# Optimization experiments

Measured on AMD Instinct MI355X. Metric: run time of the kernel, lower is better.

The kernel has to match this reference:

```python
import jax, jax.numpy as jnp
import numpy as np

NUM_EXPERTS = 8
TOP_K = 2
HIDDEN = 1024
INTER = 2048
SHARED_INTER = 1024
T = 8192
STD = 0.02


def setup_inputs() -> dict:
    key = jax.random.key(0)
    ks = jax.random.split(key, 6)
    return {
        "hidden_states": jax.random.normal(ks[0], (T, HIDDEN), dtype=jnp.float32),
        "w_gate": jax.random.normal(ks[1], (NUM_EXPERTS, HIDDEN), dtype=jnp.float32) * STD,
        "w_fc": jax.random.normal(ks[2], (NUM_EXPERTS, INTER, HIDDEN), dtype=jnp.float32) * STD,
        "w_proj": jax.random.normal(ks[3], (NUM_EXPERTS, HIDDEN, INTER), dtype=jnp.float32) * (STD / np.sqrt(2 * 24)),
        "w_fc_shared": jax.random.normal(ks[4], (SHARED_INTER, HIDDEN), dtype=jnp.float32) * STD,
        "w_proj_shared": jax.random.normal(ks[5], (HIDDEN, SHARED_INTER), dtype=jnp.float32) * (STD / np.sqrt(2 * 24)),
    }


def reference(hidden_states, w_gate, w_fc, w_proj, w_fc_shared, w_proj_shared):
    x = hidden_states.reshape(-1, HIDDEN)  # [T, d]
    # --- routing: top-k over router logits, softmax over the k selected logits (fp32) ---
    router_logits = x @ w_gate.T  # [T, E]
    top_vals, top_idx = jax.lax.top_k(router_logits, TOP_K)  # [T, K]
    gates = jax.nn.softmax(top_vals.astype(jnp.float32), axis=-1).astype(x.dtype)  # [T, K]
    # --- expert FFN: dense per-expert compute, masked combine (== scatter/grouped-GEMM math) ---
    out = jnp.zeros_like(x)
    for e in range(NUM_EXPERTS):
        gate_e = jnp.sum(jnp.where(top_idx == e, gates, jnp.zeros_like(gates)), axis=-1)  # [T]
        h = jax.nn.gelu(x @ w_fc[e].T, approximate=False) @ w_proj[e].T  # [T, d]
        out = out + gate_e[:, None] * h
    # --- shared expert ---
    shared = jax.nn.gelu(x @ w_fc_shared.T, approximate=False) @ w_proj_shared.T
    return out + shared
```

## Files before the change

kernel.cpp:

```cpp
#include <hip/hip_runtime.h>
#include <cstdint>
#include <cstdio>

#define DEVI __device__ __forceinline__

constexpr int TOKS = 8192;
constexpr int HID  = 1024;
constexpr int INTR = 2048;
constexpr int SINT = 1024;
constexpr int NEXP = 8;
constexpr int MAXSLOT = 17408;

typedef __bf16 bf16x8 __attribute__((ext_vector_type(8)));
typedef float  f32x4  __attribute__((ext_vector_type(4)));

DEVI unsigned short f2bf(float f) {
  unsigned int u = __float_as_uint(f);
  u += 0x7FFFu + ((u >> 16) & 1u);
  return (unsigned short)(u >> 16);
}

DEVI float bf2f(unsigned short h) {
  return __uint_as_float((unsigned int)h << 16);
}

DEVI void gl_lds16(const unsigned short* g, unsigned short* l) {
  __attribute__((address_space(1))) uint32_t* gp =
      (__attribute__((address_space(1))) uint32_t*)(uintptr_t)g;
  __attribute__((address_space(3))) uint32_t* lp =
      (__attribute__((address_space(3))) uint32_t*)(uint32_t)(uintptr_t)l;
  __builtin_amdgcn_global_load_lds(gp, lp, 16, 0, 0);
}

DEVI float gelu_fast(float x) {
  const float z = fabsf(x) * 0.70710678118654752f;
  const float t = __builtin_amdgcn_rcpf(1.0f + 0.3275911f * z);
  float p = 1.061405429f;
  p = p * t - 1.453152027f;
  p = p * t + 1.421413741f;
  p = p * t - 0.284496736f;
  p = p * t + 0.254829592f;
  const float e = __builtin_amdgcn_exp2f(-z * z * 1.4426950408889634f);
  float erfz = 1.0f - p * t * e;
  erfz = copysignf(erfz, x);
  return 0.5f * x * (1.0f + erfz);
}

DEVI int xcd_chunk_map(int bid, int total) {
  const int q = total >> 3, r = total & 7;
  const int x = bid & 7, i = bid >> 3;
  return (x < r ? x * (q + 1) : r * (q + 1) + (x - r) * q) + i;
}

__global__ void k_f2bf_all(const float* __restrict__ s0, unsigned short* __restrict__ d0, int n0,
                           const float* __restrict__ s1, unsigned short* __restrict__ d1, int n1,
                           const float* __restrict__ s2, unsigned short* __restrict__ d2, int n2,
                           const float* __restrict__ s3, unsigned short* __restrict__ d3, int n3) {
  const int ntot = n0 + n1 + n2 + n3;
  int i = blockIdx.x * blockDim.x + threadIdx.x;
  const int stride = gridDim.x * blockDim.x;
  for (; i < ntot; i += stride) {
    int j = i;
    const float* s; unsigned short* d;
    if (j < n0) { s = s0; d = d0; }
    else if ((j -= n0) < n1) { s = s1; d = d1; }
    else if ((j -= n1) < n2) { s = s2; d = d2; }
    else { j -= n2; s = s3; d = d3; }
    float4 v = ((const float4*)s)[j];
    ushort4 o;
    o.x = f2bf(v.x); o.y = f2bf(v.y); o.z = f2bf(v.z); o.w = f2bf(v.w);
    ((ushort4*)d)[j] = o;
  }
}

__global__ __launch_bounds__(256) void k_router(
    const float* __restrict__ x, const float* __restrict__ wg,
    unsigned short* __restrict__ xb,
    int* __restrict__ rec_e, float2* __restrict__ rec_g) {
  const int wave = threadIdx.x >> 6;
  const int lane = threadIdx.x & 63;
  const int t = blockIdx.x * 4 + wave;

  float4 xv[4];
  const float4* x4 = (const float4*)(x + (size_t)t * HID);
#pragma unroll
  for (int j = 0; j < 4; ++j) xv[j] = x4[j * 64 + lane];

  ushort4* xb4 = (ushort4*)(xb + (size_t)t * HID);
#pragma unroll
  for (int j = 0; j < 4; ++j) {
    float4 v = xv[j];
    ushort4 o; o.x = f2bf(v.x); o.y = f2bf(v.y); o.z = f2bf(v.z); o.w = f2bf(v.w);
    xb4[j * 64 + lane] = o;
  }

  float lg[NEXP];
#pragma unroll
  for (int e = 0; e < NEXP; ++e) {
    const float4* w4 = (const float4*)(wg + (size_t)e * HID);
    float s = 0.f;
#pragma unroll
    for (int j = 0; j < 4; ++j) {
      float4 a = xv[j], b = w4[j * 64 + lane];
      s += a.x * b.x + a.y * b.y + a.z * b.z + a.w * b.w;
    }
    lg[e] = s;
  }
#pragma unroll
  for (int e = 0; e < NEXP; ++e)
#pragma unroll
    for (int off = 32; off > 0; off >>= 1) lg[e] += __shfl_xor(lg[e], off);

  if (lane == 0) {
    int b0 = 0; float v0 = lg[0];
    for (int e = 1; e < NEXP; ++e) if (lg[e] > v0) { v0 = lg[e]; b0 = e; }
    int b1 = -1; float v1 = -1e30f;
    for (int e = 0; e < NEXP; ++e) if (e != b0 && lg[e] > v1) { v1 = lg[e]; b1 = e; }
    const float d = expf(v1 - v0);
    const float g0 = 1.f / (1.f + d);
    const float g1 = d / (1.f + d);
    rec_e[t] = b0 | (b1 << 16);
    rec_g[t] = make_float2(g0, g1);
  }
}

__global__ __launch_bounds__(256) void k_count(
    const int* __restrict__ rec_e, int* __restrict__ rec_p, int* __restrict__ cnt) {
  __shared__ int hist[NEXP];
  __shared__ int base[NEXP];
  const int t = blockIdx.x * 256 + threadIdx.x;
  if (threadIdx.x < NEXP) hist[threadIdx.x] = 0;
  __syncthreads();
  const int ee = rec_e[t];
  const int e0 = ee & 0xffff, e1 = ee >> 16;
  const int r0 = atomicAdd(&hist[e0], 1);
  const int r1 = atomicAdd(&hist[e1], 1);
  __syncthreads();
  if (threadIdx.x < NEXP)
    base[threadIdx.x] = atomicAdd(&cnt[threadIdx.x], hist[threadIdx.x]);
  __syncthreads();
  rec_p[t] = (base[e0] + r0) | ((base[e1] + r1) << 16);
}

__global__ void k_scan(const int* __restrict__ cnt, int* __restrict__ offs) {
  if (threadIdx.x == 0 && blockIdx.x == 0) {
    int* tb0 = offs + 16;
    int* tb1 = offs + 32;
    int o = 0, t0 = 0, t1 = 0;
    tb0[0] = 0; tb1[0] = 0;
    for (int e = 0; e < NEXP; ++e) {
      offs[e] = o;
      const int mt = (cnt[e] + 127) >> 7;
      o += mt << 7;
      t0 += mt * (INTR / 128);
      t1 += mt * (HID / 128);
      tb0[e + 1] = t0;
      tb1[e + 1] = t1;
    }
    offs[NEXP] = o;
  }
}

__global__ void k_assign(const int* __restrict__ rec_e, const int* __restrict__ rec_p,
                         const int* __restrict__ offs, int* __restrict__ tok) {
  const int t = blockIdx.x * 256 + threadIdx.x;
  if (t >= TOKS) return;
  const int ee = rec_e[t], pp = rec_p[t];
  const int s0 = offs[ee & 0xffff] + (pp & 0xffff);
  const int s1 = offs[ee >> 16] + (pp >> 16);
  tok[s0] = t;
  tok[s1] = t;
}

template <int MODE>
__global__ __launch_bounds__(256, 2) void k_gemm2(
    const unsigned short* __restrict__ A,
    const unsigned short* __restrict__ B,
    unsigned short* __restrict__ Hout,
    const int* __restrict__ cnt,
    const int* __restrict__ offs,
    const int* __restrict__ tok,
    int K, int N) {
  constexpr int NT_SHIFT = (MODE == 0) ? 4 : 3;
  constexpr int NT = 1 << NT_SHIFT;

  int count, off, e = 0, m0, n0;
  {
    int bid = blockIdx.x;
    int total;
    const int* tb = offs + ((MODE == 0) ? 16 : 32);
    if constexpr (MODE <= 1) total = tb[8];
    else                     total = (TOKS >> 7) << NT_SHIFT;
    if (bid >= total) return;
    bid = xcd_chunk_map(bid, total);
    int local;
    if constexpr (MODE <= 1) {
      while (bid >= tb[e + 1]) ++e;
      local = bid - tb[e];
      count = cnt[e]; off = offs[e];
    } else {
      local = bid; count = TOKS; off = 0;
    }
    m0 = (local >> NT_SHIFT) << 7;
    n0 = (local & (NT - 1)) << 7;
  }

  __shared__ alignas(16) unsigned short As[2][128 * 64];
  __shared__ alignas(16) unsigned short Bs[2][128 * 64];

  const int tid = threadIdx.x;
  const unsigned short* Bexp = B + ((MODE <= 1) ? (size_t)e * N * K : (size_t)0);

  const int srow = tid >> 3;
  const int schunk = tid & 7;
  const unsigned short* gA[4];
  const unsigned short* gB[4];
#pragma unroll
  for (int r = 0; r < 4; ++r) {
    const int gr = r * 32 + srow;
    int mr = m0 + gr; if (mr > count - 1) mr = count - 1;
    size_t arow;
    if (MODE == 0)      arow = (size_t)tok[off + mr] * (size_t)K;
    else if (MODE == 1) arow = (size_t)(off + mr) * (size_t)K;
    else                arow = (size_t)(m0 + gr) * (size_t)K;
    gA[r] = A + arow + (size_t)(((schunk ^ (gr & 7)) & 7) * 8);
    gB[r] = Bexp + (size_t)(n0 + gr) * (size_t)K + (size_t)(((schunk ^ (gr & 7)) & 7) * 8);
  }

  const int wid = tid >> 6;
  const int lane = tid & 63;
  const int wr = wid >> 1;
  const int wc = wid & 1;
  const int fm = lane & 15;
  const int fq = lane >> 4;
  int aOff[4], bOff[4];
#pragma unroll
  for (int i = 0; i < 4; ++i) {
    const int row = wr * 64 + i * 16 + fm;
    aOff[i] = row * 128 + ((fq ^ (row & 7)) * 16);
  }
#pragma unroll
  for (int j = 0; j < 4; ++j) {
    const int row = wc * 64 + j * 16 + fm;
    bOff[j] = row * 128 + ((fq ^ (row & 7)) * 16);
  }

  auto stage = [&](int buf, int k0) {
#pragma unroll
    for (int r = 0; r < 4; ++r)
      gl_lds16(gA[r] + k0, &As[buf][r * 2048 + tid * 8]);
#pragma unroll
    for (int r = 0; r < 4; ++r)
      gl_lds16(gB[r] + k0, &Bs[buf][r * 2048 + tid * 8]);
  };

  f32x4 acc[4][4] = {};

  stage(0, 0);
  __syncthreads();

  int cur = 0;
  for (int k0 = 0; k0 < K; k0 += 64) {
    const bool more = (k0 + 64 < K);
    if (more) stage(cur ^ 1, k0 + 64);

    const char* aBase = (const char*)&As[cur][0];
    const char* bBase = (const char*)&Bs[cur][0];
    __builtin_amdgcn_s_setprio(1);
#pragma unroll
    for (int s = 0; s < 2; ++s) {
      bf16x8 af[4], bfr[4];
#pragma unroll
      for (int i = 0; i < 4; ++i)
        af[i] = *(const bf16x8*)(aBase + (aOff[i] ^ (s << 6)));
#pragma unroll
      for (int j = 0; j < 4; ++j)
        bfr[j] = *(const bf16x8*)(bBase + (bOff[j] ^ (s << 6)));
#pragma unroll
      for (int i = 0; i < 4; ++i)
#pragma unroll
        for (int j = 0; j < 4; ++j)
          acc[i][j] = __builtin_amdgcn_mfma_f32_16x16x32_bf16(af[i], bfr[j], acc[i][j], 0, 0, 0);
    }
    __builtin_amdgcn_s_setprio(0);

    if (more) { __syncthreads(); cur ^= 1; }
  }

  constexpr bool GELU = (MODE == 0 || MODE == 2);
#pragma unroll
  for (int i = 0; i < 4; ++i) {
#pragma unroll
    for (int rr = 0; rr < 4; ++rr) {
      const int m = m0 + wr * 64 + i * 16 + fq * 4 + rr;
      if (m < count) {
        unsigned short* orow = Hout + (size_t)(off + m) * N + (n0 + wc * 64 + fm);
#pragma unroll
        for (int j = 0; j < 4; ++j) {
          const float v = acc[i][j][rr];
          orow[j * 16] = f2bf(GELU ? gelu_fast(v) : v);
        }
      }
    }
  }
}

__global__ __launch_bounds__(256) void k_combine(
    const unsigned short* __restrict__ Y,
    const unsigned short* __restrict__ Ys,
    const int* __restrict__ rec_e, const int* __restrict__ rec_p,
    const float2* __restrict__ rec_g, const int* __restrict__ offs,
    float* __restrict__ out) {
  const int t = blockIdx.x;
  const int ee = rec_e[t], pp = rec_p[t];
  const float2 g = rec_g[t];
  const int s0 = offs[ee & 0xffff] + (pp & 0xffff);
  const int s1 = offs[ee >> 16] + (pp >> 16);
  const int c = threadIdx.x * 4;
  ushort4 a = *(const ushort4*)&Y[(size_t)s0 * HID + c];
  ushort4 b = *(const ushort4*)&Y[(size_t)s1 * HID + c];
  ushort4 s = *(const ushort4*)&Ys[(size_t)t * HID + c];
  float4 o;
  o.x = g.x * bf2f(a.x) + g.y * bf2f(b.x) + bf2f(s.x);
  o.y = g.x * bf2f(a.y) + g.y * bf2f(b.y) + bf2f(s.y);
  o.z = g.x * bf2f(a.z) + g.y * bf2f(b.z) + bf2f(s.z);
  o.w = g.x * bf2f(a.w) + g.y * bf2f(b.w) + bf2f(s.w);
  *(float4*)&out[(size_t)t * HID + c] = o;
}

extern "C" void kernel_launch(void* const* d_in, const int* in_sizes, int n_in,
                              void* d_out, int out_size, void* d_ws, size_t ws_size,
                              hipStream_t stream) {
  const float* x   = (const float*)d_in[0];
  const float* wg  = (const float*)d_in[1];
  const float* wfc = (const float*)d_in[2];
  const float* wpj = (const float*)d_in[3];
  const float* wfs = (const float*)d_in[4];
  const float* wps = (const float*)d_in[5];
  float* out = (float*)d_out;
  char* ws = (char*)d_ws;

  constexpr size_t OFF_XB   = 0;
  constexpr size_t OFF_WFC  = OFF_XB   + (size_t)TOKS * HID * 2;
  constexpr size_t OFF_WPJ  = OFF_WFC  + (size_t)NEXP * INTR * HID * 2;
  constexpr size_t OFF_WFS  = OFF_WPJ  + (size_t)NEXP * HID * INTR * 2;
  constexpr size_t OFF_WPS  = OFF_WFS  + (size_t)SINT * HID * 2;
  constexpr size_t OFF_H    = OFF_WPS  + (size_t)HID * SINT * 2;
  constexpr size_t OFF_HS   = OFF_H    + (size_t)MAXSLOT * INTR * 2;
  constexpr size_t OFF_Y    = OFF_HS   + (size_t)TOKS * SINT * 2;
  constexpr size_t OFF_YS   = OFF_Y    + (size_t)MAXSLOT * HID * 2;
  constexpr size_t OFF_CNT  = OFF_YS   + (size_t)TOKS * HID * 2;
  constexpr size_t OFF_OFFS = OFF_CNT  + 32;
  constexpr size_t OFF_RECE = OFF_OFFS + 256;
  constexpr size_t OFF_RECP = OFF_RECE + (size_t)TOKS * 4;
  constexpr size_t OFF_RECG = OFF_RECP + (size_t)TOKS * 4;
  constexpr size_t OFF_TOK  = OFF_RECG + (size_t)TOKS * 8;

  unsigned short* xb   = (unsigned short*)(ws + OFF_XB);
  unsigned short* wfcb = (unsigned short*)(ws + OFF_WFC);
  unsigned short* wpjb = (unsigned short*)(ws + OFF_WPJ);
  unsigned short* wfsb = (unsigned short*)(ws + OFF_WFS);
  unsigned short* wpsb = (unsigned short*)(ws + OFF_WPS);
  unsigned short* h    = (unsigned short*)(ws + OFF_H);
  unsigned short* hs   = (unsigned short*)(ws + OFF_HS);
  unsigned short* Y    = (unsigned short*)(ws + OFF_Y);
  unsigned short* Ys   = (unsigned short*)(ws + OFF_YS);
  int*    cnt   = (int*)(ws + OFF_CNT);
  int*    offs  = (int*)(ws + OFF_OFFS);
  int*    rec_e = (int*)(ws + OFF_RECE);
  int*    rec_p = (int*)(ws + OFF_RECP);
  float2* rec_g = (float2*)(ws + OFF_RECG);
  int*    tok   = (int*)(ws + OFF_TOK);

  hipMemsetAsync(cnt, 0, NEXP * sizeof(int), stream);

  k_f2bf_all<<<2048, 256, 0, stream>>>(
      wfc, wfcb, NEXP * INTR * HID / 4,
      wpj, wpjb, NEXP * HID * INTR / 4,
      wfs, wfsb, SINT * HID / 4,
      wps, wpsb, HID * SINT / 4);

  k_router<<<TOKS / 4, 256, 0, stream>>>(x, wg, xb, rec_e, rec_g);
  k_count<<<TOKS / 256, 256, 0, stream>>>(rec_e, rec_p, cnt);
  k_scan<<<1, 64, 0, stream>>>(cnt, offs);
  k_assign<<<TOKS / 256, 256, 0, stream>>>(rec_e, rec_p, offs, tok);

  constexpr int GRID0 = 136 * (INTR / 128);
  constexpr int GRID1 = 136 * (HID / 128);
  constexpr int GRID2 = (TOKS / 128) * (SINT / 128);
  constexpr int GRID3 = (TOKS / 128) * (HID / 128);

  k_gemm2<0><<<GRID0, 256, 0, stream>>>(xb, wfcb, h, cnt, offs, tok, HID, INTR);
  k_gemm2<2><<<GRID2, 256, 0, stream>>>(xb, wfsb, hs, cnt, offs, tok, HID, SINT);
  k_gemm2<1><<<GRID1, 256, 0, stream>>>(h, wpjb, Y, cnt, offs, tok, INTR, HID);
  k_gemm2<3><<<GRID3, 256, 0, stream>>>(hs, wpsb, Ys, cnt, offs, tok, SINT, HID);

  k_combine<<<TOKS, 256, 0, stream>>>(Y, Ys, rec_e, rec_p, rec_g, offs, out);
}
```

Baseline: 442.6 us.

## Use a 4-stage K=32 LDS pipeline with explicit vmcnt waits in grouped GEMM

Replaces the double-buffered K=64 loop with a four-buffer ring of K=32 tiles, keeping three tile loads in flight through manual s_waitcnt vmcnt and raw s_barrier calls. The LDS swizzle is adapted to the 64-byte row pitch. Each step issues the next stage's loads after its fragment reads, so global-to-LDS latency overlaps the MFMA work. Total LDS size is unchanged, but the number of barriers doubles and correctness now depends on the vmcnt accounting matching the four loads issued per stage.

```diff
diff --git a/kernel.cpp b/kernel.cpp
--- a/kernel.cpp
+++ b/kernel.cpp
@@ -182,7 +182,7 @@
     const int* __restrict__ tok,
     int K, int N) {
   constexpr int NT_SHIFT = (MODE == 0) ? 4 : 3;
-  constexpr int NT = 1 << NT_SHIFT;
+  constexpr int NT_TILES = 1 << NT_SHIFT;
 
   int count, off, e = 0, m0, n0;
   {
@@ -202,29 +202,30 @@
       local = bid; count = TOKS; off = 0;
     }
     m0 = (local >> NT_SHIFT) << 7;
-    n0 = (local & (NT - 1)) << 7;
-  }
-
-  __shared__ alignas(16) unsigned short As[2][128 * 64];
-  __shared__ alignas(16) unsigned short Bs[2][128 * 64];
+    n0 = (local & (NT_TILES - 1)) << 7;
+  }
+
+  __shared__ alignas(16) unsigned short As[4][128 * 32];
+  __shared__ alignas(16) unsigned short Bs[4][128 * 32];
 
   const int tid = threadIdx.x;
   const unsigned short* Bexp = B + ((MODE <= 1) ? (size_t)e * N * K : (size_t)0);
 
-  const int srow = tid >> 3;
-  const int schunk = tid & 7;
-  const unsigned short* gA[4];
-  const unsigned short* gB[4];
-#pragma unroll
-  for (int r = 0; r < 4; ++r) {
-    const int gr = r * 32 + srow;
+  const int srow = tid >> 2;
+  const int schunk = tid & 3;
+  const unsigned short* gA[2];
+  const unsigned short* gB[2];
+#pragma unroll
+  for (int r = 0; r < 2; ++r) {
+    const int gr = r * 64 + srow;
     int mr = m0 + gr; if (mr > count - 1) mr = count - 1;
     size_t arow;
     if (MODE == 0)      arow = (size_t)tok[off + mr] * (size_t)K;
     else if (MODE == 1) arow = (size_t)(off + mr) * (size_t)K;
     else                arow = (size_t)(m0 + gr) * (size_t)K;
-    gA[r] = A + arow + (size_t)(((schunk ^ (gr & 7)) & 7) * 8);
-    gB[r] = Bexp + (size_t)(n0 + gr) * (size_t)K + (size_t)(((schunk ^ (gr & 7)) & 7) * 8);
+    const int sc = (schunk ^ ((gr >> 1) & 3)) * 8;
+    gA[r] = A + arow + (size_t)sc;
+    gB[r] = Bexp + (size_t)(n0 + gr) * (size_t)K + (size_t)sc;
   }
 
   const int wid = tid >> 6;
@@ -237,55 +238,60 @@
 #pragma unroll
   for (int i = 0; i < 4; ++i) {
     const int row = wr * 64 + i * 16 + fm;
-    aOff[i] = row * 128 + ((fq ^ (row & 7)) * 16);
+    aOff[i] = row * 64 + ((fq ^ ((row >> 1) & 3)) * 16);
   }
 #pragma unroll
   for (int j = 0; j < 4; ++j) {
     const int row = wc * 64 + j * 16 + fm;
-    bOff[j] = row * 128 + ((fq ^ (row & 7)) * 16);
+    bOff[j] = row * 64 + ((fq ^ ((row >> 1) & 3)) * 16);
   }
 
   auto stage = [&](int buf, int k0) {
-#pragma unroll
-    for (int r = 0; r < 4; ++r)
-      gl_lds16(gA[r] + k0, &As[buf][r * 2048 + tid * 8]);
-#pragma unroll
-    for (int r = 0; r < 4; ++r)
-      gl_lds16(gB[r] + k0, &Bs[buf][r * 2048 + tid * 8]);
+    gl_lds16(gA[0] + k0, &As[buf][tid * 8]);
+    gl_lds16(gA[1] + k0, &As[buf][2048 + tid * 8]);
+    gl_lds16(gB[0] + k0, &Bs[buf][tid * 8]);
+    gl_lds16(gB[1] + k0, &Bs[buf][2048 + tid * 8]);
   };
 
   f32x4 acc[4][4] = {};
 
+  auto kstep = [&](int t, bool doStage) {
+    const char* aB = (const char*)&As[t & 3][0];
+    const char* bB = (const char*)&Bs[t & 3][0];
+    bf16x8 af[4], bfr[4];
+#pragma unroll
+    for (int i = 0; i < 4; ++i) af[i] = *(const bf16x8*)(aB + aOff[i]);
+#pragma unroll
+    for (int j = 0; j < 4; ++j) bfr[j] = *(const bf16x8*)(bB + bOff[j]);
+    if (doStage) stage((t + 3) & 3, (t + 3) * 32);
+    __builtin_amdgcn_s_setprio(1);
+#pragma unroll
+    for (int i = 0; i < 4; ++i)
+#pragma unroll
+      for (int j = 0; j < 4; ++j)
+        acc[i][j] = __builtin_amdgcn_mfma_f32_16x16x32_bf16(af[i], bfr[j], acc[i][j], 0, 0, 0);
+    __builtin_amdgcn_s_setprio(0);
+  };
+
   stage(0, 0);
-  __syncthreads();
-
-  int cur = 0;
-  for (int k0 = 0; k0 < K; k0 += 64) {
-    const bool more = (k0 + 64 < K);
-    if (more) stage(cur ^ 1, k0 + 64);
-
-    const char* aBase = (const char*)&As[cur][0];
-    const char* bBase = (const char*)&Bs[cur][0];
-    __builtin_amdgcn_s_setprio(1);
-#pragma unroll
-    for (int s = 0; s < 2; ++s) {
-      bf16x8 af[4], bfr[4];
-#pragma unroll
-      for (int i = 0; i < 4; ++i)
-        af[i] = *(const bf16x8*)(aBase + (aOff[i] ^ (s << 6)));
-#pragma unroll
-      for (int j = 0; j < 4; ++j)
-        bfr[j] = *(const bf16x8*)(bBase + (bOff[j] ^ (s << 6)));
-#pragma unroll
-      for (int i = 0; i < 4; ++i)
-#pragma unroll
-        for (int j = 0; j < 4; ++j)
-          acc[i][j] = __builtin_amdgcn_mfma_f32_16x16x32_bf16(af[i], bfr[j], acc[i][j], 0, 0, 0);
-    }
-    __builtin_amdgcn_s_setprio(0);
-
-    if (more) { __syncthreads(); cur ^= 1; }
-  }
+  stage(1, 32);
+  stage(2, 64);
+
+  const int NT = K >> 5;
+  for (int t = 0; t < NT - 2; ++t) {
+    asm volatile("s_waitcnt vmcnt(8)" ::: "memory");
+    __builtin_amdgcn_s_barrier();
+    __builtin_amdgcn_sched_barrier(0);
+    kstep(t, t + 3 < NT);
+  }
+  asm volatile("s_waitcnt vmcnt(4)" ::: "memory");
+  __builtin_amdgcn_s_barrier();
+  __builtin_amdgcn_sched_barrier(0);
+  kstep(NT - 2, false);
+  asm volatile("s_waitcnt vmcnt(0)" ::: "memory");
+  __builtin_amdgcn_s_barrier();
+  __builtin_amdgcn_sched_barrier(0);
+  kstep(NT - 1, false);
 
   constexpr bool GELU = (MODE == 0 || MODE == 2);
 #pragma unroll
```

Measured after the change: 472.0 us. +6.6%, slower.
